# Kernel tuning notes

Measured on AMD Instinct MI355X. Metric: run time of the kernel, lower is better.

Reference implementation:

```python
import jax, jax.numpy as jnp
import numpy as np

B, DIM, HEADS, BLOCKS = 16, 192, 6, 6
H = W = 64
WS, SHIFT, MLP = 8, 4, 4
N = WS * WS
HD = DIM // HEADS
NW = (H // WS) * (W // WS)
SCALE = HD ** -0.5


def _ln(x, g, b, eps=1e-5):
    mu = jnp.mean(x, -1, keepdims=True)
    var = jnp.mean(jnp.square(x - mu), -1, keepdims=True)
    return (x - mu) * jax.lax.rsqrt(var + eps) * g + b


def _win_part(x):  # [B,H,W,C] -> [B*NW, N, C]
    x = x.reshape(B, H // WS, WS, W // WS, WS, DIM)
    return x.transpose(0, 1, 3, 2, 4, 5).reshape(-1, N, DIM)


def _win_rev(w):  # [B*NW, N, C] -> [B,H,W,C]
    x = w.reshape(B, H // WS, W // WS, WS, WS, DIM)
    return x.transpose(0, 1, 3, 2, 4, 5).reshape(B, H, W, DIM)


def _rel_pos_index():
    coords = np.stack(np.meshgrid(np.arange(WS), np.arange(WS), indexing='ij')).reshape(2, -1)
    rel = (coords[:, :, None] - coords[:, None, :]).transpose(1, 2, 0)
    rel[:, :, 0] += WS - 1
    rel[:, :, 1] += WS - 1
    rel[:, :, 0] *= 2 * WS - 1
    return jnp.asarray(rel.sum(-1))  # [N, N] int


def _attn_mask():  # shifted-window attention mask, [NW, N, N]
    img = np.zeros((H, W))
    cnt = 0
    for hs in (slice(0, -WS), slice(-WS, -SHIFT), slice(-SHIFT, None)):
        for ws_ in (slice(0, -WS), slice(-WS, -SHIFT), slice(-SHIFT, None)):
            img[hs, ws_] = cnt
            cnt += 1
    mw = img.reshape(H // WS, WS, W // WS, WS).transpose(0, 2, 1, 3).reshape(-1, N)
    am = mw[:, None, :] - mw[:, :, None]
    return jnp.asarray(np.where(am != 0, -100.0, 0.0).astype(np.float32))


RPI = _rel_pos_index()
MASK = _attn_mask()


def _block(x, shifted, n1g, n1b, qkvw, qkvb, pw, pb, rpb, n2g, n2b, f1w, f1b, f2w, f2b):
    shortcut = x  # [B, H*W, DIM]
    x = _ln(x, n1g, n1b).reshape(B, H, W, DIM)
    if shifted:
        x = jnp.roll(x, (-SHIFT, -SHIFT), (1, 2))
    xw = _win_part(x)  # [B*NW, N, DIM]
    qkv = (xw @ qkvw.T + qkvb).reshape(-1, N, 3, HEADS, HD).transpose(2, 0, 3, 1, 4)
    q, k, v = qkv[0], qkv[1], qkv[2]  # [B*NW, HEADS, N, HD]
    attn = jnp.einsum('bhnd,bhmd->bhnm', q * SCALE, k)
    attn = attn + rpb[RPI].transpose(2, 0, 1)[None]  # relative position bias
    if shifted:
        attn = (attn.reshape(B, NW, HEADS, N, N) + MASK[None, :, None]).reshape(-1, HEADS, N, N)
    attn = jax.nn.softmax(attn, -1)
    xw = jnp.einsum('bhnm,bhmd->bnhd', attn, v).reshape(-1, N, DIM)
    xw = xw @ pw.T + pb
    x = _win_rev(xw)
    if shifted:
        x = jnp.roll(x, (SHIFT, SHIFT), (1, 2))
    x = shortcut + x.reshape(B, H * W, DIM)
    h = _ln(x, n2g, n2b)
    h = jax.nn.gelu(h @ f1w.T + f1b, approximate=False) @ f2w.T + f2b
    return x + h


def _forward(x, en_g, en_b, n1_g, n1_b, qkv_w, qkv_b, proj_w, proj_b, rpb, n2_g, n2_b, fc1_w, fc1_b, fc2_w, fc2_b, fn_g, fn_b, conv_w):
    y = x.reshape(B, DIM, H * W).transpose(0, 2, 1)  # patch embed (patch_size=1)
    y = _ln(y, en_g, en_b)
    for i in range(BLOCKS):
        y = _block(y, i % 2 == 1, n1_g[i], n1_b[i], qkv_w[i], qkv_b[i], proj_w[i], proj_b[i],
                   rpb[i], n2_g[i], n2_b[i], fc1_w[i], fc1_b[i], fc2_w[i], fc2_b[i])
    y = _ln(y, fn_g, fn_b)
    y = y.transpose(0, 2, 1).reshape(B, DIM, H, W)  # patch unembed
    return y + jax.lax.conv_general_dilated(y, conv_w, (1, 1), 'SAME',
                                            dimension_numbers=('NCHW', 'OIHW', 'NCHW'))


def setup_inputs() -> dict:
    key = jax.random.key(0)
    ks = jax.random.split(key, 7)
    s = 0.02
    f32 = jnp.float32
    return {
        'x': jax.random.normal(ks[0], (B, DIM, H, W), f32),
        'en_g': jnp.ones((DIM,), f32), 'en_b': jnp.zeros((DIM,), f32),
        'n1_g': jnp.ones((BLOCKS, DIM), f32), 'n1_b': jnp.zeros((BLOCKS, DIM), f32),
        'qkv_w': s * jax.random.normal(ks[1], (BLOCKS, 3 * DIM, DIM), f32),
        'qkv_b': jnp.zeros((BLOCKS, 3 * DIM), f32),
        'proj_w': s * jax.random.normal(ks[2], (BLOCKS, DIM, DIM), f32),
        'proj_b': jnp.zeros((BLOCKS, DIM), f32),
        'rpb': s * jax.random.normal(ks[3], (BLOCKS, (2 * WS - 1) ** 2, HEADS), f32),
        'n2_g': jnp.ones((BLOCKS, DIM), f32), 'n2_b': jnp.zeros((BLOCKS, DIM), f32),
        'fc1_w': s * jax.random.normal(ks[4], (BLOCKS, MLP * DIM, DIM), f32),
        'fc1_b': jnp.zeros((BLOCKS, MLP * DIM), f32),
        'fc2_w': s * jax.random.normal(ks[5], (BLOCKS, DIM, MLP * DIM), f32),
        'fc2_b': jnp.zeros((BLOCKS, DIM), f32),
        'fn_g': jnp.ones((DIM,), f32), 'fn_b': jnp.zeros((DIM,), f32),
        'conv_w': s * jax.random.normal(ks[6], (DIM, DIM, 3, 3), f32),
    }


def reference(x, en_g, en_b, n1_g, n1_b, qkv_w, qkv_b, proj_w, proj_b, rpb, n2_g, n2_b, fc1_w, fc1_b, fc2_w, fc2_b, fn_g, fn_b, conv_w):
    return _forward(x, en_g, en_b, n1_g, n1_b, qkv_w, qkv_b, proj_w, proj_b, rpb,
                    n2_g, n2_b, fc1_w, fc1_b, fc2_w, fc2_b, fn_g, fn_b, conv_w)
```

## Files before the change

kernel.cpp:

```cpp
#include <hip/hip_runtime.h>
#include <cstdint>
#include <cstddef>

#define BATCH 16
#define DIM 192
#define HEADS 6
#define HD 32
#define TOK 65536
#define QKV_D 576
#define MLP_D 768
#define SCALE 0.17677669529663687f

#define CH 32768

typedef __bf16 bf16x8 __attribute__((ext_vector_type(8)));
typedef float f32x4 __attribute__((ext_vector_type(4)));

__device__ __forceinline__ unsigned short f2bf(float f) {
  union { float f; unsigned u; } c;
  c.f = f;
  return (unsigned short)((c.u + 0x7fffu + ((c.u >> 16) & 1)) >> 16);
}

__device__ __forceinline__ float waveSum(float v) {
#pragma unroll
  for (int off = 32; off; off >>= 1) v += __shfl_xor(v, off, 64);
  return v;
}

__device__ __forceinline__ float rowSum16(float v) {
  v += __shfl_xor(v, 1, 64);
  v += __shfl_xor(v, 2, 64);
  v += __shfl_xor(v, 4, 64);
  v += __shfl_xor(v, 8, 64);
  return v;
}

#define GLD(SRC, DST)                                                     \
  __builtin_amdgcn_global_load_lds(                                       \
      (const __attribute__((address_space(1))) void*)(SRC),               \
      (__attribute__((address_space(3))) void*)(DST), 16, 0, 0)

__global__ __launch_bounds__(64) void zero_k(float* p) { p[threadIdx.x] = 0.f; }

__global__ __launch_bounds__(256) void cvt_k(const float* __restrict__ s,
                                             unsigned short* __restrict__ d,
                                             int n) {
  int i = ((blockIdx.x << 8) + threadIdx.x) << 2;
  if (i < n) {
    float4 v = *(const float4*)(s + i);
    d[i] = f2bf(v.x);
    d[i + 1] = f2bf(v.y);
    d[i + 2] = f2bf(v.z);
    d[i + 3] = f2bf(v.w);
  }
}

__global__ __launch_bounds__(256) void cvt_qkv_k(const float* __restrict__ s,
                                                 unsigned short* __restrict__ d) {
  int i = (blockIdx.x << 8) + threadIdx.x;
  if (i < 663552) {
    int r = (i / 192) % 576;
    float v = s[i];
    if (r < 192) v *= SCALE;
    d[i] = f2bf(v);
  }
}

__global__ __launch_bounds__(256) void scale_qkvb_k(const float* __restrict__ s,
                                                    float* __restrict__ d) {
  int i = (blockIdx.x << 8) + threadIdx.x;
  if (i < 3456) {
    float v = s[i];
    if ((i % 576) < 192) v *= SCALE;
    d[i] = v;
  }
}

__global__ __launch_bounds__(256) void cvt_conv_k(const float* __restrict__ s,
                                                  unsigned short* __restrict__ d) {
  int i = (blockIdx.x << 8) + threadIdx.x;
  if (i < 331776) {
    int o = i / 1728;
    int r = i - o * 1728;
    int tap = r / 192;
    int ci = r - tap * 192;
    d[i] = f2bf(s[o * 1728 + ci * 9 + tap]);
  }
}

__global__ __launch_bounds__(256) void embed_ln_t_k(
    const float* __restrict__ x, const float* __restrict__ g,
    const float* __restrict__ be, float* __restrict__ y) {
  __shared__ float ts[192 * 65];
  const int w = threadIdx.x >> 6, lane = threadIdx.x & 63;
  const int t0 = blockIdx.x << 6;
  const int b = t0 >> 12, tb = t0 & 4095;
  const float* xb = x + (((size_t)b * DIM) << 12) + tb;
#pragma unroll
  for (int j = 0; j < 48; ++j) {
    int ch = w * 48 + j;
    ts[ch * 65 + lane] = xb[((size_t)ch << 12) + lane];
  }
  __syncthreads();
#pragma unroll 4
  for (int idx = 0; idx < 16; ++idx) {
    int tk = (w << 4) + idx;
    float v0 = ts[lane * 65 + tk];
    float v1 = ts[(lane + 64) * 65 + tk];
    float v2 = ts[(lane + 128) * 65 + tk];
    float mu = waveSum(v0 + v1 + v2) * (1.f / 192.f);
    float d0 = v0 - mu, d1 = v1 - mu, d2 = v2 - mu;
    float var = waveSum(d0 * d0 + d1 * d1 + d2 * d2) * (1.f / 192.f);
    float rs = rsqrtf(var + 1e-5f);
    float* yp = y + (size_t)(t0 + tk) * DIM;
    yp[lane] = d0 * rs * g[lane] + be[lane];
    yp[lane + 64] = d1 * rs * g[lane + 64] + be[lane + 64];
    yp[lane + 128] = d2 * rs * g[lane + 128] + be[lane + 128];
  }
}

__global__ __launch_bounds__(256) void ln_final_k(
    float* __restrict__ y, const float* __restrict__ g,
    const float* __restrict__ be, unsigned short* __restrict__ hb) {
  int tok = (blockIdx.x << 2) + (threadIdx.x >> 6);
  int lane = threadIdx.x & 63;
  float* yp = y + (size_t)tok * DIM;
  float v0 = yp[lane], v1 = yp[lane + 64], v2 = yp[lane + 128];
  float mu = waveSum(v0 + v1 + v2) * (1.f / 192.f);
  float d0 = v0 - mu, d1 = v1 - mu, d2 = v2 - mu;
  float var = waveSum(d0 * d0 + d1 * d1 + d2 * d2) * (1.f / 192.f);
  float rs = rsqrtf(var + 1e-5f);
  float r0 = d0 * rs * g[lane] + be[lane];
  float r1 = d1 * rs * g[lane + 64] + be[lane + 64];
  float r2 = d2 * rs * g[lane + 128] + be[lane + 128];
  yp[lane] = r0;
  yp[lane + 64] = r1;
  yp[lane + 128] = r2;
  unsigned short* op = hb + (size_t)tok * DIM;
  op[lane] = f2bf(r0);
  op[lane + 64] = f2bf(r1);
  op[lane + 128] = f2bf(r2);
}

__global__ __launch_bounds__(256) void ln_window_k(
    const float* __restrict__ y, const float* __restrict__ g,
    const float* __restrict__ be, unsigned short* __restrict__ xw,
    int shifted) {
  int m = (blockIdx.x << 2) + (threadIdx.x >> 6);
  int lane = threadIdx.x & 63;
  int widx = m >> 6, n = m & 63;
  int b = widx >> 6, win = widx & 63;
  int hp = ((win >> 3) << 3) + (n >> 3);
  int wp = ((win & 7) << 3) + (n & 7);
  if (shifted) { hp = (hp + 4) & 63; wp = (wp + 4) & 63; }
  int src = (b << 12) + (hp << 6) + wp;
  const float* yp = y + (size_t)src * DIM;
  float v0 = yp[lane], v1 = yp[lane + 64], v2 = yp[lane + 128];
  float mu = waveSum(v0 + v1 + v2) * (1.f / 192.f);
  float d0 = v0 - mu, d1 = v1 - mu, d2 = v2 - mu;
  float var = waveSum(d0 * d0 + d1 * d1 + d2 * d2) * (1.f / 192.f);
  float rs = rsqrtf(var + 1e-5f);
  unsigned short* op = xw + (size_t)m * DIM;
  op[lane] = f2bf(d0 * rs * g[lane] + be[lane]);
  op[lane + 64] = f2bf(d1 * rs * g[lane + 64] + be[lane + 64]);
  op[lane + 128] = f2bf(d2 * rs * g[lane + 128] + be[lane + 128]);
}

__global__ __launch_bounds__(64) void attn_k(
    const unsigned short* __restrict__ qkv, const float* __restrict__ rpb,
    unsigned short* __restrict__ out, int shifted, int widx0) {
  __shared__ unsigned short vt[32 * 72];
  __shared__ unsigned short pl[64 * 72];
  __shared__ float rp[228];
  const int lwidx = blockIdx.x / HEADS;
  const int head = blockIdx.x - lwidx * HEADS;
  const int l = threadIdx.x;
  const int g = l >> 4, li = l & 15;

  for (int i = l; i < 225; i += 64) rp[i] = rpb[i * HEADS + head];

  const unsigned short* base = qkv + (size_t)lwidx * 64 * QKV_D + head * HD;

  bf16x8 qf[4], kf[4];
#pragma unroll
  for (int n = 0; n < 4; ++n)
    qf[n] = *(const bf16x8*)(base + (size_t)(16 * n + li) * QKV_D + g * 8);
#pragma unroll
  for (int i = 0; i < 4; ++i)
    kf[i] = *(const bf16x8*)(base + (size_t)(16 * i + li) * QKV_D + DIM + g * 8);

#pragma unroll
  for (int p = 0; p < 4; ++p) {
    int r = 16 * p + (l >> 2);
    int d0 = (l & 3) << 3;
    bf16x8 v8 = *(const bf16x8*)(base + (size_t)r * QKV_D + 2 * DIM + d0);
#pragma unroll
    for (int e = 0; e < 8; ++e)
      vt[(d0 + e) * 72 + r] = ((const unsigned short*)&v8)[e];
  }

  f32x4 s[4][4] = {};
#pragma unroll
  for (int i = 0; i < 4; ++i)
#pragma unroll
    for (int n = 0; n < 4; ++n)
      s[i][n] = __builtin_amdgcn_mfma_f32_16x16x32_bf16(kf[i], qf[n], s[i][n],
                                                        0, 0, 0);
  __syncthreads();

  const int win = (widx0 + lwidx) & 63;
  const int wh = (win >> 3) << 3, wwp = (win & 7) << 3;
  int rq[4], cq[4], zq[4];
#pragma unroll
  for (int n = 0; n < 4; ++n) {
    int q = 16 * n + li;
    rq[n] = q >> 3;
    cq[n] = q & 7;
    zq[n] = 0;
    if (shifted) {
      int hq = wh + rq[n], wq = wwp + cq[n];
      int zr = hq < 56 ? 0 : (hq < 60 ? 1 : 2);
      int zc = wq < 56 ? 0 : (wq < 60 ? 1 : 2);
      zq[n] = 3 * zr + zc;
    }
  }
#pragma unroll
  for (int i = 0; i < 4; ++i)
#pragma unroll
    for (int j = 0; j < 4; ++j) {
      int m = 16 * i + 4 * g + j;
      int rm = m >> 3, cm = m & 7;
      int zm = 0;
      if (shifted) {
        int hm = wh + rm, wm = wwp + cm;
        int zr = hm < 56 ? 0 : (hm < 60 ? 1 : 2);
        int zc = wm < 56 ? 0 : (wm < 60 ? 1 : 2);
        zm = 3 * zr + zc;
      }
#pragma unroll
      for (int n = 0; n < 4; ++n) {
        float b = rp[(rq[n] - rm + 7) * 15 + (cq[n] - cm + 7)];
        if (shifted && zm != zq[n]) b -= 100.f;
        s[i][n][j] += b;
      }
    }

  float inv[4];
#pragma unroll
  for (int n = 0; n < 4; ++n) {
    float m0 = -1e30f;
#pragma unroll
    for (int i = 0; i < 4; ++i)
#pragma unroll
      for (int j = 0; j < 4; ++j) m0 = fmaxf(m0, s[i][n][j]);
    m0 = fmaxf(m0, __shfl_xor(m0, 16, 64));
    m0 = fmaxf(m0, __shfl_xor(m0, 32, 64));
    float s0 = 0.f;
#pragma unroll
    for (int i = 0; i < 4; ++i)
#pragma unroll
      for (int j = 0; j < 4; ++j) {
        float e = __expf(s[i][n][j] - m0);
        s[i][n][j] = e;
        s0 += e;
      }
    s0 += __shfl_xor(s0, 16, 64);
    s0 += __shfl_xor(s0, 32, 64);
    inv[n] = 1.f / s0;
  }

#pragma unroll
  for (int n = 0; n < 4; ++n) {
    int q = 16 * n + li;
#pragma unroll
    for (int i = 0; i < 4; ++i) {
      unsigned lo = (unsigned)f2bf(s[i][n][0]) | ((unsigned)f2bf(s[i][n][1]) << 16);
      unsigned hi = (unsigned)f2bf(s[i][n][2]) | ((unsigned)f2bf(s[i][n][3]) << 16);
      *(uint2*)&pl[q * 72 + 16 * i + 4 * g] = uint2{lo, hi};
    }
  }
  __syncthreads();

  f32x4 o[2][4] = {};
#pragma unroll
  for (int ks = 0; ks < 2; ++ks) {
    bf16x8 va[2], pb[4];
#pragma unroll
    for (int i2 = 0; i2 < 2; ++i2)
      va[i2] = *(const bf16x8*)&vt[(16 * i2 + li) * 72 + 32 * ks + 8 * g];
#pragma unroll
    for (int n2 = 0; n2 < 4; ++n2)
      pb[n2] = *(const bf16x8*)&pl[(16 * n2 + li) * 72 + 32 * ks + 8 * g];
#pragma unroll
    for (int i2 = 0; i2 < 2; ++i2)
#pragma unroll
      for (int n2 = 0; n2 < 4; ++n2)
        o[i2][n2] = __builtin_amdgcn_mfma_f32_16x16x32_bf16(va[i2], pb[n2],
                                                            o[i2][n2], 0, 0, 0);
  }

  unsigned short* ob = out + (size_t)(lwidx * 64) * DIM + head * HD;
#pragma unroll
  for (int i2 = 0; i2 < 2; ++i2)
#pragma unroll
    for (int n2 = 0; n2 < 4; ++n2) {
      int q = 16 * n2 + li;
      float iv = inv[n2];
      unsigned lo = (unsigned)f2bf(o[i2][n2][0] * iv) |
                    ((unsigned)f2bf(o[i2][n2][1] * iv) << 16);
      unsigned hi = (unsigned)f2bf(o[i2][n2][2] * iv) |
                    ((unsigned)f2bf(o[i2][n2][3] * iv) << 16);
      *(uint2*)(ob + (size_t)q * DIM + 16 * i2 + 4 * g) = uint2{lo, hi};
    }
}

__device__ __forceinline__ void mfma_block256(const unsigned short* As,
                                              const unsigned short* Bs,
                                              f32x4 acc[4][4], int w,
                                              int lane) {
  const int frow = lane & 15;
  const int fk = (lane >> 4) << 3;
#pragma unroll
  for (int kk = 0; kk < 64; kk += 32) {
    int slotk = (kk + fk) >> 3;
    bf16x8 a[4], b[4];
#pragma unroll
    for (int m = 0; m < 4; ++m) {
      int ar = (w << 6) + (m << 4) + frow;
      a[m] = *(const bf16x8*)&As[(ar << 6) + ((slotk ^ (ar & 7)) << 3)];
    }
#pragma unroll
    for (int n = 0; n < 4; ++n) {
      int br = (n << 4) + frow;
      b[n] = *(const bf16x8*)&Bs[(br << 6) + ((slotk ^ (br & 7)) << 3)];
    }
#pragma unroll
    for (int m = 0; m < 4; ++m)
#pragma unroll
      for (int n = 0; n < 4; ++n)
        acc[m][n] =
            __builtin_amdgcn_mfma_f32_16x16x32_bf16(a[m], b[n], acc[m][n], 0,
                                                    0, 0);
  }
}

__device__ __forceinline__ void mfma_block128(const unsigned short* As,
                                              const unsigned short* Bs,
                                              f32x4 acc[2][4], int w,
                                              int lane) {
  const int frow = lane & 15;
  const int fk = (lane >> 4) << 3;
#pragma unroll
  for (int kk = 0; kk < 64; kk += 32) {
    int slotk = (kk + fk) >> 3;
    int ar0 = (w << 5) + frow, ar1 = ar0 + 16;
    bf16x8 a0 = *(const bf16x8*)&As[(ar0 << 6) + ((slotk ^ (ar0 & 7)) << 3)];
    bf16x8 a1 = *(const bf16x8*)&As[(ar1 << 6) + ((slotk ^ (ar1 & 7)) << 3)];
    bf16x8 b[4];
#pragma unroll
    for (int n = 0; n < 4; ++n) {
      int br = (n << 4) + frow;
      b[n] = *(const bf16x8*)&Bs[(br << 6) + ((slotk ^ (br & 7)) << 3)];
    }
#pragma unroll
    for (int n = 0; n < 4; ++n) {
      acc[0][n] = __builtin_amdgcn_mfma_f32_16x16x32_bf16(a0, b[n], acc[0][n], 0, 0, 0);
      acc[1][n] = __builtin_amdgcn_mfma_f32_16x16x32_bf16(a1, b[n], acc[1][n], 0, 0, 0);
    }
  }
}

template <int EPI>
__global__ __launch_bounds__(256) void mgemm_k(
    const unsigned short* __restrict__ A, const unsigned short* __restrict__ W,
    const float* __restrict__ bias, void* __restrict__ Cv, int N, int K) {
  __shared__ unsigned short As[256 * 64];
  __shared__ unsigned short Bs[64 * 64];
  const int tid = threadIdx.x;
  const int w = tid >> 6, lane = tid & 63;
  const int row0 = blockIdx.x << 8;
  const int col0 = blockIdx.y << 6;
  f32x4 acc[4][4] = {};

  for (int k0 = 0; k0 < K; k0 += 64) {
    if (k0) __syncthreads();
#pragma unroll
    for (int r = 0; r < 2; ++r) {
      int q = (r << 8) + tid;
      int brow = q >> 3, cs = q & 7;
      int kg = cs ^ (brow & 7);
      GLD(W + (size_t)(col0 + brow) * K + k0 + (kg << 3),
          Bs + (((r << 8) + (w << 6)) << 3));
    }
#pragma unroll
    for (int r = 0; r < 8; ++r) {
      int q = (r << 8) + tid;
      int arow = q >> 3, cs = q & 7;
      int kg = cs ^ (arow & 7);
      GLD(A + (size_t)(row0 + arow) * K + k0 + (kg << 3),
          As + (((r << 8) + (w << 6)) << 3));
    }
    __syncthreads();
    mfma_block256(As, Bs, acc, w, lane);
  }

  const int erow = (lane >> 4) << 2;
  const int ecol = lane & 15;
#pragma unroll
  for (int mr = 0; mr < 4; ++mr)
#pragma unroll
    for (int nr = 0; nr < 4; ++nr)
#pragma unroll
      for (int j = 0; j < 4; ++j) {
        int row = row0 + (w << 6) + (mr << 4) + erow + j;
        int col = col0 + (nr << 4) + ecol;
        float v = acc[mr][nr][j];
        ((unsigned short*)Cv)[(size_t)row * N + col] = f2bf(v + bias[col]);
      }
}

__global__ __launch_bounds__(256) void wgemm_k(
    const unsigned short* __restrict__ A, const unsigned short* __restrict__ W,
    const float* __restrict__ bias, float* __restrict__ y,
    unsigned short* __restrict__ lnout, const float* __restrict__ g,
    const float* __restrict__ be, int K, int sh2) {
  __shared__ unsigned short As[64 * 64];
  __shared__ unsigned short Bs[192 * 64];
  const int tid = threadIdx.x;
  const int w = tid >> 6, lane = tid & 63;
  const int row0 = blockIdx.x << 6;
  f32x4 acc[12] = {};

  for (int k0 = 0; k0 < K; k0 += 64) {
    if (k0) __syncthreads();
#pragma unroll
    for (int r = 0; r < 6; ++r) {
      int q = (r << 8) + tid;
      int brow = q >> 3, cs = q & 7;
      int kg = cs ^ (brow & 7);
      GLD(W + (size_t)brow * K + k0 + (kg << 3),
          Bs + (((r << 8) + (w << 6)) << 3));
    }
#pragma unroll
    for (int r = 0; r < 2; ++r) {
      int q = (r << 8) + tid;
      int arow = q >> 3, cs = q & 7;
      int kg = cs ^ (arow & 7);
      GLD(A + (size_t)(row0 + arow) * K + k0 + (kg << 3),
          As + (((r << 8) + (w << 6)) << 3));
    }
    __syncthreads();
    const int frow = lane & 15;
    const int fk = (lane >> 4) << 3;
#pragma unroll
    for (int kk = 0; kk < 64; kk += 32) {
      int slotk = (kk + fk) >> 3;
      int ar = (w << 4) + frow;
      bf16x8 a = *(const bf16x8*)&As[(ar << 6) + ((slotk ^ (ar & 7)) << 3)];
      bf16x8 b[12];
#pragma unroll
      for (int n = 0; n < 12; ++n) {
        int br = (n << 4) + frow;
        b[n] = *(const bf16x8*)&Bs[(br << 6) + ((slotk ^ (br & 7)) << 3)];
      }
#pragma unroll
      for (int n = 0; n < 12; ++n)
        acc[n] = __builtin_amdgcn_mfma_f32_16x16x32_bf16(a, b[n], acc[n], 0, 0,
                                                         0);
    }
  }

  const int erow = (lane >> 4) << 2;
  const int ecol = lane & 15;
  float bv[12], gv[12], bev[12];
#pragma unroll
  for (int n = 0; n < 12; ++n) {
    int col = (n << 4) + ecol;
    bv[n] = bias[col];
    gv[n] = g[col];
    bev[n] = be[col];
  }

#pragma unroll
  for (int j = 0; j < 4; ++j) {
    int m = row0 + (w << 4) + erow + j;
    int n64 = m & 63, widx = m >> 6;
    int bl = widx >> 6, win = widx & 63;
    int hp = ((win >> 3) << 3) + (n64 >> 3);
    int wp = ((win & 7) << 3) + (n64 & 7);
    if (sh2) { hp = (hp + 4) & 63; wp = (wp + 4) & 63; }
    int tok = (bl << 12) + (hp << 6) + wp;
    float* yp = y + (size_t)tok * DIM;
    float v[12];
    float s0 = 0.f;
#pragma unroll
    for (int n = 0; n < 12; ++n) {
      v[n] = acc[n][j] + bv[n] + yp[(n << 4) + ecol];
      s0 += v[n];
    }
#pragma unroll
    for (int n = 0; n < 12; ++n) yp[(n << 4) + ecol] = v[n];
    float mu = rowSum16(s0) * (1.f / 192.f);
    float s1 = 0.f;
#pragma unroll
    for (int n = 0; n < 12; ++n) {
      float d = v[n] - mu;
      s1 += d * d;
    }
    float rs = rsqrtf(rowSum16(s1) * (1.f / 192.f) + 1e-5f);
    unsigned short* op = lnout + (size_t)tok * DIM;
#pragma unroll
    for (int n = 0; n < 12; ++n)
      op[(n << 4) + ecol] = f2bf((v[n] - mu) * rs * gv[n] + bev[n]);
  }
}

template <int LAST>
__global__ __launch_bounds__(256) void mlp_k(
    const unsigned short* __restrict__ A, const unsigned short* __restrict__ W1,
    const float* __restrict__ b1, const unsigned short* __restrict__ W2,
    const float* __restrict__ b2, float* __restrict__ y,
    unsigned short* __restrict__ lnout, const float* __restrict__ g,
    const float* __restrict__ be, int sh2) {
  __shared__ unsigned short As[64 * 192];
  __shared__ unsigned short Wb1[64 * 192];
  __shared__ unsigned short Wb2[192 * 64];
  __shared__ unsigned short hc[64 * 64];
  const int tid = threadIdx.x;
  const int w = tid >> 6, lane = tid & 63;
  const int row0 = blockIdx.x << 6;
  const int frow = lane & 15;
  const int fk = (lane >> 4) << 3;
  const int erow = (lane >> 4) << 2;
  const int ecol = lane & 15;

#pragma unroll
  for (int r = 0; r < 6; ++r) {
    int q = (r << 8) + tid;
    int kb = q >> 9, row = (q >> 3) & 63, cs = q & 7;
    int kg = cs ^ (row & 7);
    GLD(A + (size_t)(row0 + row) * 192 + kb * 64 + (kg << 3),
        As + (((r << 8) + (w << 6)) << 3));
  }

  f32x4 acc2[12] = {};

  for (int n0 = 0; n0 < 12; ++n0) {
    __syncthreads();
#pragma unroll
    for (int r = 0; r < 6; ++r) {
      int q = (r << 8) + tid;
      int kb = q >> 9, row = (q >> 3) & 63, cs = q & 7;
      int kg = cs ^ (row & 7);
      GLD(W1 + (size_t)(n0 * 64 + row) * 192 + kb * 64 + (kg << 3),
          Wb1 + (((r << 8) + (w << 6)) << 3));
    }
#pragma unroll
    for (int r = 0; r < 6; ++r) {
      int q = (r << 8) + tid;
      int row = q >> 3, cs = q & 7;
      int kg = cs ^ (row & 7);
      GLD(W2 + (size_t)row * 768 + n0 * 64 + (kg << 3),
          Wb2 + (((r << 8) + (w << 6)) << 3));
    }
    __syncthreads();
    f32x4 acc1[4] = {};
#pragma unroll
    for (int kk = 0; kk < 192; kk += 32) {
      int kb = kk >> 6;
      int slotk = ((kk & 63) + fk) >> 3;
      int ar = (w << 4) + frow;
      bf16x8 a = *(const bf16x8*)&As[(kb << 12) + (ar << 6) +
                                     ((slotk ^ (ar & 7)) << 3)];
#pragma unroll
      for (int n = 0; n < 4; ++n) {
        int br = (n << 4) + frow;
        bf16x8 b = *(const bf16x8*)&Wb1[(kb << 12) + (br << 6) +
                                        ((slotk ^ (br & 7)) << 3)];
        acc1[n] = __builtin_amdgcn_mfma_f32_16x16x32_bf16(a, b, acc1[n], 0, 0, 0);
      }
    }
#pragma unroll
    for (int n = 0; n < 4; ++n) {
      float bb = b1[n0 * 64 + (n << 4) + ecol];
#pragma unroll
      for (int j = 0; j < 4; ++j) {
        int hr = (w << 4) + erow + j;
        int hcol = (n << 4) + ecol;
        float xg = acc1[n][j] + bb;
        float x3 = xg * xg * xg;
        float t1 = fmaf(0.044715f, x3, xg);
        float e = __expf(t1 * -1.5957691216057308f);
        float hv = xg * __builtin_amdgcn_rcpf(1.f + e);
        hc[(hr << 6) + (((hcol >> 3) ^ (hr & 7)) << 3) + (hcol & 7)] = f2bf(hv);
      }
    }
#pragma unroll
    for (int kk = 0; kk < 64; kk += 32) {
      int slotk = (kk + fk) >> 3;
      int ar = (w << 4) + frow;
      bf16x8 a = *(const bf16x8*)&hc[(ar << 6) + ((slotk ^ (ar & 7)) << 3)];
#pragma unroll
      for (int n = 0; n < 12; ++n) {
        int br = (n << 4) + frow;
        bf16x8 b = *(const bf16x8*)&Wb2[(br << 6) + ((slotk ^ (br & 7)) << 3)];
        acc2[n] = __builtin_amdgcn_mfma_f32_16x16x32_bf16(a, b, acc2[n], 0, 0, 0);
      }
    }
  }

  float bv[12], gv[12], bev[12];
#pragma unroll
  for (int n = 0; n < 12; ++n) {
    int col = (n << 4) + ecol;
    bv[n] = b2[col];
    if (LAST == 0) { gv[n] = g[col]; bev[n] = be[col]; }
  }

#pragma unroll
  for (int j = 0; j < 4; ++j) {
    int tok = row0 + (w << 4) + erow + j;
    float* yp = y + (size_t)tok * DIM;
    float v[12];
    float s0 = 0.f;
#pragma unroll
    for (int n = 0; n < 12; ++n) {
      v[n] = acc2[n][j] + bv[n] + yp[(n << 4) + ecol];
      s0 += v[n];
    }
#pragma unroll
    for (int n = 0; n < 12; ++n) yp[(n << 4) + ecol] = v[n];
    if (LAST == 0) {
      float mu = rowSum16(s0) * (1.f / 192.f);
      float s1 = 0.f;
#pragma unroll
      for (int n = 0; n < 12; ++n) {
        float d = v[n] - mu;
        s1 += d * d;
      }
      float rs = rsqrtf(rowSum16(s1) * (1.f / 192.f) + 1e-5f);
      int hw = tok & 4095;
      int gi = tok >> 12;
      int h = hw >> 6, ww = hw & 63;
      int hs = sh2 ? (h + 60) & 63 : h;
      int ws = sh2 ? (ww + 60) & 63 : ww;
      int win = ((hs >> 3) << 3) | (ws >> 3);
      int n64 = ((hs & 7) << 3) | (ws & 7);
      size_t drow = ((size_t)gi << 12) + (win << 6) + n64;
      unsigned short* op = lnout + drow * DIM;
#pragma unroll
      for (int n = 0; n < 12; ++n)
        op[(n << 4) + ecol] = f2bf((v[n] - mu) * rs * gv[n] + bev[n]);
    }
  }
}

__global__ __launch_bounds__(256) void conv_k(
    const unsigned short* __restrict__ A, const unsigned short* __restrict__ W,
    float* __restrict__ out, const float* __restrict__ Z,
    const unsigned short* __restrict__ zpg) {
  __shared__ unsigned short As[128 * 64];
  __shared__ unsigned short Bs[64 * 64];
  const int tid = threadIdx.x;
  const int w = tid >> 6, lane = tid & 63;
  const int row0 = blockIdx.x << 7;
  const int col0 = blockIdx.y << 6;
  f32x4 acc[2][4] = {};
  bool first = true;

#pragma unroll
  for (int tap = 0; tap < 9; ++tap) {
    const int dh = tap / 3 - 1, dw = tap % 3 - 1;
#pragma unroll
    for (int k0 = 0; k0 < 192; k0 += 64) {
      if (!first) __syncthreads();
      first = false;
#pragma unroll
      for (int r = 0; r < 2; ++r) {
        int q = (r << 8) + tid;
        int brow = q >> 3, cs = q & 7;
        int kg = cs ^ (brow & 7);
        GLD(W + (size_t)(col0 + brow) * 1728 + tap * 192 + k0 + (kg << 3),
            Bs + (((r << 8) + (w << 6)) << 3));
      }
#pragma unroll
      for (int r = 0; r < 4; ++r) {
        int q = (r << 8) + tid;
        int arow = q >> 3, cs = q & 7;
        int kg = cs ^ (arow & 7);
        int m = row0 + arow;
        int hw_ = m & 4095;
        int h = hw_ >> 6, ww = hw_ & 63;
        int ih = h + dh, iw = ww + dw;
        const unsigned short* src =
            ((unsigned)ih < 64u && (unsigned)iw < 64u)
                ? A + (size_t)(m + dh * 64 + dw) * DIM + k0 + (kg << 3)
                : zpg;
        GLD(src, As + (((r << 8) + (w << 6)) << 3));
      }
      __syncthreads();
      mfma_block128(As, Bs, acc, w, lane);
    }
  }

  const int erow = (lane >> 4) << 2;
  const int ecol = lane & 15;
#pragma unroll
  for (int mr = 0; mr < 2; ++mr)
#pragma unroll
    for (int nr = 0; nr < 4; ++nr)
#pragma unroll
      for (int j = 0; j < 4; ++j) {
        int row = row0 + (w << 5) + (mr << 4) + erow + j;
        int col = col0 + (nr << 4) + ecol;
        int b = row >> 12, hw_ = row & 4095;
        out[(((size_t)(b * DIM + col)) << 12) + hw_] =
            acc[mr][nr][j] + Z[(size_t)row * DIM + col];
      }
}

extern "C" void kernel_launch(void* const* d_in, const int* in_sizes, int n_in,
                              void* d_out, int out_size, void* d_ws,
                              size_t ws_size, hipStream_t stream) {
  const float* x = (const float*)d_in[0];
  const float* en_g = (const float*)d_in[1];
  const float* en_b = (const float*)d_in[2];
  const float* n1_g = (const float*)d_in[3];
  const float* n1_b = (const float*)d_in[4];
  const float* qkv_w = (const float*)d_in[5];
  const float* qkv_b = (const float*)d_in[6];
  const float* proj_w = (const float*)d_in[7];
  const float* proj_b = (const float*)d_in[8];
  const float* rpb = (const float*)d_in[9];
  const float* n2_g = (const float*)d_in[10];
  const float* n2_b = (const float*)d_in[11];
  const float* fc1_w = (const float*)d_in[12];
  const float* fc1_b = (const float*)d_in[13];
  const float* fc2_w = (const float*)d_in[14];
  const float* fc2_b = (const float*)d_in[15];
  const float* fn_g = (const float*)d_in[16];
  const float* fn_b = (const float*)d_in[17];
  const float* conv_w = (const float*)d_in[18];
  float* out = (float*)d_out;

  float* y = (float*)d_ws;
  unsigned short* buf1 = (unsigned short*)((char*)d_ws + 50331648);
  unsigned short* buf2u = (unsigned short*)((char*)d_ws + 75497472);
  unsigned short* ln2buf = buf2u;
  unsigned short* wbuf = (unsigned short*)((char*)d_ws + 113246208);
  unsigned short* zpg = (unsigned short*)((char*)d_ws + 119218176);
  float* qkv_bs = (float*)((char*)d_ws + 119218432);

  unsigned short* qkv_wb = wbuf;
  unsigned short* proj_wb = wbuf + 663552;
  unsigned short* fc1_wb = wbuf + 884736;
  unsigned short* fc2_wb = wbuf + 1769472;
  unsigned short* conv_wb = wbuf + 2654208;

  zero_k<<<1, 64, 0, stream>>>((float*)zpg);
  cvt_qkv_k<<<2592, 256, 0, stream>>>(qkv_w, qkv_wb);
  scale_qkvb_k<<<14, 256, 0, stream>>>(qkv_b, qkv_bs);
  cvt_k<<<216, 256, 0, stream>>>(proj_w, proj_wb, 221184);
  cvt_k<<<864, 256, 0, stream>>>(fc1_w, fc1_wb, 884736);
  cvt_k<<<864, 256, 0, stream>>>(fc2_w, fc2_wb, 884736);
  cvt_conv_k<<<1296, 256, 0, stream>>>(conv_w, conv_wb);

  embed_ln_t_k<<<1024, 256, 0, stream>>>(x, en_g, en_b, y);
  ln_window_k<<<16384, 256, 0, stream>>>(y, n1_g, n1_b, buf1, 0);

  for (int i = 0; i < 6; ++i) {
    int sh = i & 1;
    for (int c = 0; c < 2; ++c) {
      unsigned short* b1c = buf1 + (size_t)c * CH * DIM;
      mgemm_k<3><<<dim3(CH / 256, 9), 256, 0, stream>>>(
          b1c, qkv_wb + (size_t)i * QKV_D * DIM, qkv_bs + i * QKV_D, buf2u,
          QKV_D, DIM);
      attn_k<<<(CH / 64) * HEADS, 64, 0, stream>>>(
          buf2u, rpb + i * 225 * HEADS, b1c, sh, c * (CH / 64));
    }
    wgemm_k<<<TOK / 64, 256, 0, stream>>>(
        buf1, proj_wb + (size_t)i * DIM * DIM, proj_b + i * DIM, y, ln2buf,
        n2_g + i * DIM, n2_b + i * DIM, DIM, sh);
    if (i < 5) {
      mlp_k<0><<<TOK / 64, 256, 0, stream>>>(
          ln2buf, fc1_wb + (size_t)i * MLP_D * DIM, fc1_b + i * MLP_D,
          fc2_wb + (size_t)i * DIM * MLP_D, fc2_b + i * DIM, y, buf1,
          n1_g + (i + 1) * DIM, n1_b + (i + 1) * DIM, (i + 1) & 1);
    } else {
      mlp_k<1><<<TOK / 64, 256, 0, stream>>>(
          ln2buf, fc1_wb + (size_t)i * MLP_D * DIM, fc1_b + i * MLP_D,
          fc2_wb + (size_t)i * DIM * MLP_D, fc2_b + i * DIM, y, buf1, fn_g,
          fn_b, 0);
    }
  }

  ln_final_k<<<16384, 256, 0, stream>>>(y, fn_g, fn_b, buf1);
  conv_k<<<dim3(TOK / 128, 3), 256, 0, stream>>>(buf1, conv_wb, out, y, zpg);
}
```

Baseline: 1.268 ms.

## Fuse attention projection, residual and LayerNorm2 into the MLP kernel

Merges the separate projection GEMM (wgemm_k) into the MLP kernel. The proj output plus residual is LayerNormed straight into shared memory and fed to fc1 without a global round trip. The residual is kept in registers, so y is read once and written once per block instead of twice each, and the tokens are mapped back from window order at the end. Ping-pong window buffers and a four-way QKV chunking are added, which raises register and shared-memory pressure in the fused kernel.

Measured after the change: 1.386 ms. +9.3%, slower.

```diff
diff --git a/kernel.cpp b/kernel.cpp
--- a/kernel.cpp
+++ b/kernel.cpp
@@ -11,7 +11,7 @@
 #define MLP_D 768
 #define SCALE 0.17677669529663687f
 
-#define CH 32768
+#define CHQ 16384
 
 typedef __bf16 bf16x8 __attribute__((ext_vector_type(8)));
 typedef float f32x4 __attribute__((ext_vector_type(4)));
@@ -420,110 +420,16 @@
       }
 }
 
-__global__ __launch_bounds__(256) void wgemm_k(
-    const unsigned short* __restrict__ A, const unsigned short* __restrict__ W,
-    const float* __restrict__ bias, float* __restrict__ y,
-    unsigned short* __restrict__ lnout, const float* __restrict__ g,
-    const float* __restrict__ be, int K, int sh2) {
-  __shared__ unsigned short As[64 * 64];
-  __shared__ unsigned short Bs[192 * 64];
-  const int tid = threadIdx.x;
-  const int w = tid >> 6, lane = tid & 63;
-  const int row0 = blockIdx.x << 6;
-  f32x4 acc[12] = {};
-
-  for (int k0 = 0; k0 < K; k0 += 64) {
-    if (k0) __syncthreads();
-#pragma unroll
-    for (int r = 0; r < 6; ++r) {
-      int q = (r << 8) + tid;
-      int brow = q >> 3, cs = q & 7;
-      int kg = cs ^ (brow & 7);
-      GLD(W + (size_t)brow * K + k0 + (kg << 3),
-          Bs + (((r << 8) + (w << 6)) << 3));
-    }
-#pragma unroll
-    for (int r = 0; r < 2; ++r) {
-      int q = (r << 8) + tid;
-      int arow = q >> 3, cs = q & 7;
-      int kg = cs ^ (arow & 7);
-      GLD(A + (size_t)(row0 + arow) * K + k0 + (kg << 3),
-          As + (((r << 8) + (w << 6)) << 3));
-    }
-    __syncthreads();
-    const int frow = lane & 15;
-    const int fk = (lane >> 4) << 3;
-#pragma unroll
-    for (int kk = 0; kk < 64; kk += 32) {
-      int slotk = (kk + fk) >> 3;
-      int ar = (w << 4) + frow;
-      bf16x8 a = *(const bf16x8*)&As[(ar << 6) + ((slotk ^ (ar & 7)) << 3)];
-      bf16x8 b[12];
-#pragma unroll
-      for (int n = 0; n < 12; ++n) {
-        int br = (n << 4) + frow;
-        b[n] = *(const bf16x8*)&Bs[(br << 6) + ((slotk ^ (br & 7)) << 3)];
-      }
-#pragma unroll
-      for (int n = 0; n < 12; ++n)
-        acc[n] = __builtin_amdgcn_mfma_f32_16x16x32_bf16(a, b[n], acc[n], 0, 0,
-                                                         0);
-    }
-  }
-
-  const int erow = (lane >> 4) << 2;
-  const int ecol = lane & 15;
-  float bv[12], gv[12], bev[12];
-#pragma unroll
-  for (int n = 0; n < 12; ++n) {
-    int col = (n << 4) + ecol;
-    bv[n] = bias[col];
-    gv[n] = g[col];
-    bev[n] = be[col];
-  }
-
-#pragma unroll
-  for (int j = 0; j < 4; ++j) {
-    int m = row0 + (w << 4) + erow + j;
-    int n64 = m & 63, widx = m >> 6;
-    int bl = widx >> 6, win = widx & 63;
-    int hp = ((win >> 3) << 3) + (n64 >> 3);
-    int wp = ((win & 7) << 3) + (n64 & 7);
-    if (sh2) { hp = (hp + 4) & 63; wp = (wp + 4) & 63; }
-    int tok = (bl << 12) + (hp << 6) + wp;
-    float* yp = y + (size_t)tok * DIM;
-    float v[12];
-    float s0 = 0.f;
-#pragma unroll
-    for (int n = 0; n < 12; ++n) {
-      v[n] = acc[n][j] + bv[n] + yp[(n << 4) + ecol];
-      s0 += v[n];
-    }
-#pragma unroll
-    for (int n = 0; n < 12; ++n) yp[(n << 4) + ecol] = v[n];
-    float mu = rowSum16(s0) * (1.f / 192.f);
-    float s1 = 0.f;
-#pragma unroll
-    for (int n = 0; n < 12; ++n) {
-      float d = v[n] - mu;
-      s1 += d * d;
-    }
-    float rs = rsqrtf(rowSum16(s1) * (1.f / 192.f) + 1e-5f);
-    unsigned short* op = lnout + (size_t)tok * DIM;
-#pragma unroll
-    for (int n = 0; n < 12; ++n)
-      op[(n << 4) + ecol] = f2bf((v[n] - mu) * rs * gv[n] + bev[n]);
-  }
-}
-
 template <int LAST>
-__global__ __launch_bounds__(256) void mlp_k(
-    const unsigned short* __restrict__ A, const unsigned short* __restrict__ W1,
+__global__ __launch_bounds__(256) void pm_k(
+    const unsigned short* __restrict__ A, const unsigned short* __restrict__ Wp,
+    const float* __restrict__ bp, const float* __restrict__ g2,
+    const float* __restrict__ be2, const unsigned short* __restrict__ W1,
     const float* __restrict__ b1, const unsigned short* __restrict__ W2,
     const float* __restrict__ b2, float* __restrict__ y,
-    unsigned short* __restrict__ lnout, const float* __restrict__ g,
-    const float* __restrict__ be, int sh2) {
-  __shared__ unsigned short As[64 * 192];
+    unsigned short* __restrict__ lnout, const float* __restrict__ g1,
+    const float* __restrict__ be1, int sh_cur, int sh_next) {
+  __shared__ unsigned short a2[64 * 192];
   __shared__ unsigned short Wb1[64 * 192];
   __shared__ unsigned short Wb2[192 * 64];
   __shared__ unsigned short hc[64 * 64];
@@ -535,33 +441,115 @@
   const int erow = (lane >> 4) << 2;
   const int ecol = lane & 15;
 
-#pragma unroll
-  for (int r = 0; r < 6; ++r) {
-    int q = (r << 8) + tid;
-    int kb = q >> 9, row = (q >> 3) & 63, cs = q & 7;
-    int kg = cs ^ (row & 7);
-    GLD(A + (size_t)(row0 + row) * 192 + kb * 64 + (kg << 3),
-        As + (((r << 8) + (w << 6)) << 3));
+  bf16x8 ap[6];
+  {
+    const unsigned short* arp = A + (size_t)(row0 + (w << 4) + frow) * 192 + fk;
+#pragma unroll
+    for (int t = 0; t < 6; ++t) ap[t] = *(const bf16x8*)(arp + t * 32);
+  }
+
+  f32x4 accp[12] = {};
+#pragma unroll
+  for (int k0 = 0; k0 < 192; k0 += 64) {
+    __syncthreads();
+#pragma unroll
+    for (int r = 0; r < 6; ++r) {
+      int q = (r << 8) + tid;
+      int rw = q >> 3, cs = q & 7;
+      int kg = cs ^ (rw & 7);
+      GLD(Wp + (size_t)rw * 192 + k0 + (kg << 3),
+          Wb2 + (((r << 8) + (w << 6)) << 3));
+    }
+    __syncthreads();
+#pragma unroll
+    for (int kk2 = 0; kk2 < 64; kk2 += 32) {
+      int slotk = (kk2 + fk) >> 3;
+      int t = (k0 + kk2) >> 5;
+#pragma unroll
+      for (int n = 0; n < 12; ++n) {
+        int br = (n << 4) + frow;
+        bf16x8 b = *(const bf16x8*)&Wb2[(br << 6) + ((slotk ^ (br & 7)) << 3)];
+        accp[n] =
+            __builtin_amdgcn_mfma_f32_16x16x32_bf16(ap[t], b, accp[n], 0, 0, 0);
+      }
+    }
+  }
+
+  int tokj[4];
+  {
+    float bpv[12], gv2[12], bv2[12];
+#pragma unroll
+    for (int n = 0; n < 12; ++n) {
+      int col = (n << 4) + ecol;
+      bpv[n] = bp[col];
+      gv2[n] = g2[col];
+      bv2[n] = be2[col];
+    }
+#pragma unroll
+    for (int j = 0; j < 4; ++j) {
+      int m = row0 + (w << 4) + erow + j;
+      int n64 = m & 63, widx = m >> 6;
+      int bl = widx >> 6, win = widx & 63;
+      int hp = ((win >> 3) << 3) + (n64 >> 3);
+      int wp2 = ((win & 7) << 3) + (n64 & 7);
+      if (sh_cur) { hp = (hp + 4) & 63; wp2 = (wp2 + 4) & 63; }
+      int tok = (bl << 12) + (hp << 6) + wp2;
+      tokj[j] = tok;
+      const float* yp = y + (size_t)tok * DIM;
+      float s0 = 0.f;
+#pragma unroll
+      for (int n = 0; n < 12; ++n) {
+        float v = accp[n][j] + bpv[n] + yp[(n << 4) + ecol];
+        accp[n][j] = v;
+        s0 += v;
+      }
+      float mu = rowSum16(s0) * (1.f / 192.f);
+      float s1 = 0.f;
+#pragma unroll
+      for (int n = 0; n < 12; ++n) {
+        float d = accp[n][j] - mu;
+        s1 += d * d;
+      }
+      float rs = rsqrtf(rowSum16(s1) * (1.f / 192.f) + 1e-5f);
+      int hr = (w << 4) + erow + j;
+#pragma unroll
+      for (int n = 0; n < 12; ++n) {
+        int col = (n << 4) + ecol;
+        unsigned short lv = f2bf((accp[n][j] - mu) * rs * gv2[n] + bv2[n]);
+        int kb = col >> 6, c64 = col & 63;
+        a2[(kb << 12) + (hr << 6) + (((c64 >> 3) ^ (hr & 7)) << 3) + (c64 & 7)] =
+            lv;
+      }
+    }
+  }
+  {
+    int ar = (w << 4) + frow;
+#pragma unroll
+    for (int t = 0; t < 6; ++t) {
+      int kb = t >> 1;
+      int slotk = (((t & 1) << 5) + fk) >> 3;
+      ap[t] = *(const bf16x8*)&a2[(kb << 12) + (ar << 6) +
+                                  ((slotk ^ (ar & 7)) << 3)];
+    }
   }
 
   f32x4 acc2[12] = {};
-
   for (int n0 = 0; n0 < 12; ++n0) {
     __syncthreads();
 #pragma unroll
     for (int r = 0; r < 6; ++r) {
       int q = (r << 8) + tid;
-      int kb = q >> 9, row = (q >> 3) & 63, cs = q & 7;
-      int kg = cs ^ (row & 7);
-      GLD(W1 + (size_t)(n0 * 64 + row) * 192 + kb * 64 + (kg << 3),
+      int kb = q >> 9, rw = (q >> 3) & 63, cs = q & 7;
+      int kg = cs ^ (rw & 7);
+      GLD(W1 + (size_t)(n0 * 64 + rw) * 192 + kb * 64 + (kg << 3),
           Wb1 + (((r << 8) + (w << 6)) << 3));
     }
 #pragma unroll
     for (int r = 0; r < 6; ++r) {
       int q = (r << 8) + tid;
-      int row = q >> 3, cs = q & 7;
-      int kg = cs ^ (row & 7);
-      GLD(W2 + (size_t)row * 768 + n0 * 64 + (kg << 3),
+      int rw = q >> 3, cs = q & 7;
+      int kg = cs ^ (rw & 7);
+      GLD(W2 + (size_t)rw * 768 + n0 * 64 + (kg << 3),
           Wb2 + (((r << 8) + (w << 6)) << 3));
     }
     __syncthreads();
@@ -570,15 +558,13 @@
     for (int kk = 0; kk < 192; kk += 32) {
       int kb = kk >> 6;
       int slotk = ((kk & 63) + fk) >> 3;
-      int ar = (w << 4) + frow;
-      bf16x8 a = *(const bf16x8*)&As[(kb << 12) + (ar << 6) +
-                                     ((slotk ^ (ar & 7)) << 3)];
 #pragma unroll
       for (int n = 0; n < 4; ++n) {
         int br = (n << 4) + frow;
         bf16x8 b = *(const bf16x8*)&Wb1[(kb << 12) + (br << 6) +
                                         ((slotk ^ (br & 7)) << 3)];
-        acc1[n] = __builtin_amdgcn_mfma_f32_16x16x32_bf16(a, b, acc1[n], 0, 0, 0);
+        acc1[n] = __builtin_amdgcn_mfma_f32_16x16x32_bf16(ap[kk >> 5], b,
+                                                          acc1[n], 0, 0, 0);
       }
     }
 #pragma unroll
@@ -605,28 +591,28 @@
       for (int n = 0; n < 12; ++n) {
         int br = (n << 4) + frow;
         bf16x8 b = *(const bf16x8*)&Wb2[(br << 6) + ((slotk ^ (br & 7)) << 3)];
-        acc2[n] = __builtin_amdgcn_mfma_f32_16x16x32_bf16(a, b, acc2[n], 0, 0, 0);
-      }
-    }
-  }
-
-  float bv[12], gv[12], bev[12];
+        acc2[n] =
+            __builtin_amdgcn_mfma_f32_16x16x32_bf16(a, b, acc2[n], 0, 0, 0);
+      }
+    }
+  }
+
+  float b2v[12], gv[12], bev[12];
 #pragma unroll
   for (int n = 0; n < 12; ++n) {
     int col = (n << 4) + ecol;
-    bv[n] = b2[col];
-    if (LAST == 0) { gv[n] = g[col]; bev[n] = be[col]; }
-  }
-
+    b2v[n] = b2[col];
+    if (LAST == 0) { gv[n] = g1[col]; bev[n] = be1[col]; }
+  }
 #pragma unroll
   for (int j = 0; j < 4; ++j) {
-    int tok = row0 + (w << 4) + erow + j;
+    int tok = tokj[j];
     float* yp = y + (size_t)tok * DIM;
     float v[12];
     float s0 = 0.f;
 #pragma unroll
     for (int n = 0; n < 12; ++n) {
-      v[n] = acc2[n][j] + bv[n] + yp[(n << 4) + ecol];
+      v[n] = accp[n][j] + acc2[n][j] + b2v[n];
       s0 += v[n];
     }
 #pragma unroll
@@ -640,11 +626,10 @@
         s1 += d * d;
       }
       float rs = rsqrtf(rowSum16(s1) * (1.f / 192.f) + 1e-5f);
-      int hw = tok & 4095;
-      int gi = tok >> 12;
-      int h = hw >> 6, ww = hw & 63;
-      int hs = sh2 ? (h + 60) & 63 : h;
-      int ws = sh2 ? (ww + 60) & 63 : ww;
+      int hw = tok & 4095, gi = tok >> 12;
+      int h = hw >> 6, ww2 = hw & 63;
+      int hs = sh_next ? (h + 60) & 63 : h;
+      int ws = sh_next ? (ww2 + 60) & 63 : ww2;
       int win = ((hs >> 3) << 3) | (ws >> 3);
       int n64 = ((hs & 7) << 3) | (ws & 7);
       size_t drow = ((size_t)gi << 12) + (win << 6) + n64;
@@ -745,12 +730,12 @@
   float* out = (float*)d_out;
 
   float* y = (float*)d_ws;
-  unsigned short* buf1 = (unsigned short*)((char*)d_ws + 50331648);
-  unsigned short* buf2u = (unsigned short*)((char*)d_ws + 75497472);
-  unsigned short* ln2buf = buf2u;
-  unsigned short* wbuf = (unsigned short*)((char*)d_ws + 113246208);
-  unsigned short* zpg = (unsigned short*)((char*)d_ws + 119218176);
-  float* qkv_bs = (float*)((char*)d_ws + 119218432);
+  unsigned short* buf1a = (unsigned short*)((char*)d_ws + 50331648);
+  unsigned short* qkvbuf = (unsigned short*)((char*)d_ws + 75497472);
+  unsigned short* buf1b = (unsigned short*)((char*)d_ws + 94371840);
+  unsigned short* wbuf = (unsigned short*)((char*)d_ws + 119537664);
+  unsigned short* zpg = (unsigned short*)((char*)d_ws + 125509632);
+  float* qkv_bs = (float*)((char*)d_ws + 125509888);
 
   unsigned short* qkv_wb = wbuf;
   unsigned short* proj_wb = wbuf + 663552;
@@ -767,34 +752,35 @@
   cvt_conv_k<<<1296, 256, 0, stream>>>(conv_w, conv_wb);
 
   embed_ln_t_k<<<1024, 256, 0, stream>>>(x, en_g, en_b, y);
-  ln_window_k<<<16384, 256, 0, stream>>>(y, n1_g, n1_b, buf1, 0);
+  ln_window_k<<<16384, 256, 0, stream>>>(y, n1_g, n1_b, buf1a, 0);
 
   for (int i = 0; i < 6; ++i) {
     int sh = i & 1;
-    for (int c = 0; c < 2; ++c) {
-      unsigned short* b1c = buf1 + (size_t)c * CH * DIM;
-      mgemm_k<3><<<dim3(CH / 256, 9), 256, 0, stream>>>(
-          b1c, qkv_wb + (size_t)i * QKV_D * DIM, qkv_bs + i * QKV_D, buf2u,
+    unsigned short* bufA = (i & 1) ? buf1b : buf1a;
+    unsigned short* bufB = (i & 1) ? buf1a : buf1b;
+    for (int c = 0; c < 4; ++c) {
+      unsigned short* bAc = bufA + (size_t)c * CHQ * DIM;
+      mgemm_k<3><<<dim3(CHQ / 256, 9), 256, 0, stream>>>(
+          bAc, qkv_wb + (size_t)i * QKV_D * DIM, qkv_bs + i * QKV_D, qkvbuf,
           QKV_D, DIM);
-      attn_k<<<(CH / 64) * HEADS, 64, 0, stream>>>(
-          buf2u, rpb + i * 225 * HEADS, b1c, sh, c * (CH / 64));
-    }
-    wgemm_k<<<TOK / 64, 256, 0, stream>>>(
-        buf1, proj_wb + (size_t)i * DIM * DIM, proj_b + i * DIM, y, ln2buf,
-        n2_g + i * DIM, n2_b + i * DIM, DIM, sh);
+      attn_k<<<(CHQ / 64) * HEADS, 64, 0, stream>>>(
+          qkvbuf, rpb + i * 225 * HEADS, bAc, sh, c * (CHQ / 64));
+    }
     if (i < 5) {
-      mlp_k<0><<<TOK / 64, 256, 0, stream>>>(
-          ln2buf, fc1_wb + (size_t)i * MLP_D * DIM, fc1_b + i * MLP_D,
-          fc2_wb + (size_t)i * DIM * MLP_D, fc2_b + i * DIM, y, buf1,
-          n1_g + (i + 1) * DIM, n1_b + (i + 1) * DIM, (i + 1) & 1);
+      pm_k<0><<<TOK / 64, 256, 0, stream>>>(
+          bufA, proj_wb + (size_t)i * DIM * DIM, proj_b + i * DIM,
+          n2_g + i * DIM, n2_b + i * DIM, fc1_wb + (size_t)i * MLP_D * DIM,
+          fc1_b + i * MLP_D, fc2_wb + (size_t)i * DIM * MLP_D, fc2_b + i * DIM,
+          y, bufB, n1_g + (i + 1) * DIM, n1_b + (i + 1) * DIM, sh, (i + 1) & 1);
     } else {
-      mlp_k<1><<<TOK / 64, 256, 0, stream>>>(
-          ln2buf, fc1_wb + (size_t)i * MLP_D * DIM, fc1_b + i * MLP_D,
-          fc2_wb + (size_t)i * DIM * MLP_D, fc2_b + i * DIM, y, buf1, fn_g,
-          fn_b, 0);
-    }
-  }
-
-  ln_final_k<<<16384, 256, 0, stream>>>(y, fn_g, fn_b, buf1);
-  conv_k<<<dim3(TOK / 128, 3), 256, 0, stream>>>(buf1, conv_wb, out, y, zpg);
-}
+      pm_k<1><<<TOK / 64, 256, 0, stream>>>(
+          bufA, proj_wb + (size_t)i * DIM * DIM, proj_b + i * DIM,
+          n2_g + i * DIM, n2_b + i * DIM, fc1_wb + (size_t)i * MLP_D * DIM,
+          fc1_b + i * MLP_D, fc2_wb + (size_t)i * DIM * MLP_D, fc2_b + i * DIM,
+          y, bufB, fn_g, fn_b, sh, 0);
+    }
+  }
+
+  ln_final_k<<<16384, 256, 0, stream>>>(y, fn_g, fn_b, buf1a);
+  conv_k<<<dim3(TOK / 128, 3), 256, 0, stream>>>(buf1a, conv_wb, out, y, zpg);
+}
```
